# Performance work log

Measured on AMD Instinct MI355X. Metric: run time of the kernel, lower is better.

Reference implementation:

```python
import jax, jax.numpy as jnp
import numpy as np

KP_EXTENT = 0.05
N_Q = 40000   # query points
N_S = 40000   # support points
K = 32        # neighbors per query
P = 15        # kernel points
IN_DIM = 64
OUT_DIM = 128


def setup_inputs() -> dict:
    key = jax.random.key(0)
    k1, k2, k3, k4, k5, k6 = jax.random.split(key, 6)
    q_pts = jax.random.uniform(k1, (N_Q, 3), dtype=jnp.float32)
    s_pts = jax.random.uniform(k2, (N_S, 3), dtype=jnp.float32)
    # indices in [0, N_S]; value N_S hits the appended shadow row
    neighbor_idxs = jax.random.randint(k3, (N_Q, K), 0, N_S + 1)
    x = jax.random.normal(k4, (N_S, IN_DIM), dtype=jnp.float32)
    weights = jax.random.normal(k5, (P, IN_DIM, OUT_DIM), dtype=jnp.float32) * 0.05
    kernel_points = jax.random.normal(k6, (P, 3), dtype=jnp.float32) * 0.06
    return {"q_pts": q_pts, "s_pts": s_pts, "neighbor_idxs": neighbor_idxs,
            "x": x, "weights": weights, "kernel_points": kernel_points}


def reference(q_pts, s_pts, neighbor_idxs, x, weights, kernel_points):
    # Append shadow support point. NOTE: the original does
    # zeros_like(s_pts[:1,:] + 1e6) which is exactly zeros, so shadow = origin.
    s_pad = jnp.concatenate([s_pts, jnp.zeros_like(s_pts[:1, :])], axis=0)
    # Gather neighbor coordinates, center on queries: [N, K, 3]
    neighbors = s_pad[neighbor_idxs] - q_pts[:, None, :]
    # Distances to every kernel point: [N, K, P]
    diff = neighbors[:, :, None, :] - kernel_points[None, None, :, :]
    sq_distances = jnp.sum(diff * diff, axis=3)
    all_weights = jnp.clip(1.0 - jnp.sqrt(sq_distances) / KP_EXTENT, 0.0)
    all_weights = jnp.transpose(all_weights, (0, 2, 1))  # [N, P, K]
    # Gather neighbor features with zero shadow row: [N, K, D_in]
    feats = jnp.concatenate([x, jnp.zeros_like(x[:1, :])], axis=0)
    neighbors_x = feats[neighbor_idxs]
    # Kernel-point weighted aggregation: [N, P, D_in] -> [P, N, D_in]
    weighted_features = jnp.transpose(jnp.matmul(all_weights, neighbors_x), (1, 0, 2))
    # Per-kernel-point linear map: [P, N, D_out], then sum over kernel points
    kernel_outputs = jnp.matmul(weighted_features, weights)
    output_features = jnp.sum(kernel_outputs, axis=0)  # [N, D_out]
    # Normalize by count of "valid" neighbors (feature-sum > 0 heuristic)
    neighbor_features_sum = jnp.sum(neighbors_x, axis=-1)          # [N, K]
    neighbor_num = jnp.sum(neighbor_features_sum > 0.0, axis=-1)   # [N]
    neighbor_num = jnp.maximum(neighbor_num, 1).astype(output_features.dtype)
    return output_features / neighbor_num[:, None]
```

## Files before the change

### kernel.cpp

```cpp
#include <hip/hip_runtime.h>

#define N_Q     40000
#define N_S     40000
#define KK      32
#define PP      15
#define IN_DIM  64
#define OUT_DIM 128

__global__ __launch_bounds__(256) void rowsum_valid_kernel(
    const float* __restrict__ x, int* __restrict__ valid) {
  int t = blockIdx.x * 256 + threadIdx.x;
  int row = t >> 4;
  int sub = t & 15;
  if (row >= N_S) return;
  float4 v = reinterpret_cast<const float4*>(x + (size_t)row * IN_DIM)[sub];
  float s = (v.x + v.y) + (v.z + v.w);
  s += __shfl_xor(s, 1, 64);
  s += __shfl_xor(s, 2, 64);
  s += __shfl_xor(s, 4, 64);
  s += __shfl_xor(s, 8, 64);
  if (sub == 0) valid[row] = (s > 0.0f) ? 1 : 0;
}

__global__ __launch_bounds__(256) void kpconv_kernel(
    const float* __restrict__ q_pts, const float* __restrict__ s_pts,
    const int* __restrict__ nidx, const float* __restrict__ x,
    const float* __restrict__ weights, const float* __restrict__ kpts,
    const int* __restrict__ valid, float* __restrict__ out) {
  __shared__ float s_wf[4][PP * IN_DIM];
  __shared__ float s_nbr[4][KK * 3];
  __shared__ int   s_idx[4][KK];
  __shared__ int   s_pmask[4];
  __shared__ float s_kp[PP * 3];

  const int wave = threadIdx.x >> 6;
  const int lane = threadIdx.x & 63;
  const int n = blockIdx.x * 4 + wave;

  if (threadIdx.x < PP * 3) s_kp[threadIdx.x] = kpts[threadIdx.x];
  float* wf = s_wf[wave];
  for (int i = lane; i < PP * IN_DIM; i += 64) wf[i] = 0.0f;
  if (lane == 0) s_pmask[wave] = 0;

  const float qx = q_pts[n * 3 + 0];
  const float qy = q_pts[n * 3 + 1];
  const float qz = q_pts[n * 3 + 2];

  int cnt = 0;
  if (lane < KK) {
    int id = nidx[(size_t)n * KK + lane];
    s_idx[wave][lane] = id;
    float sx = 0.f, sy = 0.f, sz = 0.f;
    if (id < N_S) {
      sx = s_pts[id * 3 + 0];
      sy = s_pts[id * 3 + 1];
      sz = s_pts[id * 3 + 2];
      cnt = valid[id];
    }
    s_nbr[wave][lane * 3 + 0] = sx - qx;
    s_nbr[wave][lane * 3 + 1] = sy - qy;
    s_nbr[wave][lane * 3 + 2] = sz - qz;
  }
  unsigned long long bal = __ballot(cnt);
  int num = (int)__popcll(bal);
  if (num < 1) num = 1;
  const float fnum = (float)num;

  __syncthreads();

  for (int i = lane; i < PP * KK; i += 64) {
    const int p = i >> 5;
    const int k = i & 31;
    const float dx = s_nbr[wave][k * 3 + 0] - s_kp[p * 3 + 0];
    const float dy = s_nbr[wave][k * 3 + 1] - s_kp[p * 3 + 1];
    const float dz = s_nbr[wave][k * 3 + 2] - s_kp[p * 3 + 2];
    const float d2 = dx * dx + dy * dy + dz * dz;
    const float w = 1.0f - sqrtf(d2) * 20.0f;
    const int id = s_idx[wave][k];
    if (w > 0.0f && id < N_S) {
      atomicOr(&s_pmask[wave], 1 << p);
      const float4* f = reinterpret_cast<const float4*>(x + (size_t)id * IN_DIM);
      float* dst = wf + p * IN_DIM;
      #pragma unroll 4
      for (int d4 = 0; d4 < IN_DIM / 4; ++d4) {
        float4 v = f[d4];
        atomicAdd(&dst[d4 * 4 + 0], w * v.x);
        atomicAdd(&dst[d4 * 4 + 1], w * v.y);
        atomicAdd(&dst[d4 * 4 + 2], w * v.z);
        atomicAdd(&dst[d4 * 4 + 3], w * v.w);
      }
    }
  }
  __syncthreads();

  float acc0 = 0.f, acc1 = 0.f;
  int pmask = s_pmask[wave];
  const int o = lane * 2;
  while (pmask) {
    const int p = __ffs(pmask) - 1;
    pmask &= pmask - 1;
    const float* wp = weights + (size_t)p * IN_DIM * OUT_DIM + o;
    const float* wfp = wf + p * IN_DIM;
    #pragma unroll 8
    for (int d = 0; d < IN_DIM; ++d) {
      const float c = wfp[d];
      const float2 w2 = *reinterpret_cast<const float2*>(wp + (size_t)d * OUT_DIM);
      acc0 += c * w2.x;
      acc1 += c * w2.y;
    }
  }
  float2 res;
  res.x = acc0 / fnum;
  res.y = acc1 / fnum;
  *reinterpret_cast<float2*>(out + (size_t)n * OUT_DIM + o) = res;
}

extern "C" void kernel_launch(void* const* d_in, const int* in_sizes, int n_in,
                              void* d_out, int out_size, void* d_ws, size_t ws_size,
                              hipStream_t stream) {
  const float* q_pts   = (const float*)d_in[0];
  const float* s_pts   = (const float*)d_in[1];
  const int*   nidx    = (const int*)d_in[2];
  const float* x       = (const float*)d_in[3];
  const float* weights = (const float*)d_in[4];
  const float* kpts    = (const float*)d_in[5];
  float* out = (float*)d_out;
  int* valid = (int*)d_ws;

  rowsum_valid_kernel<<<(N_S * 16) / 256, 256, 0, stream>>>(x, valid);
  kpconv_kernel<<<N_Q / 4, 256, 0, stream>>>(q_pts, s_pts, nidx, x, weights,
                                             kpts, valid, out);
}
```

Measured before the change: 122.5 us.

## Parallelize over neighbor pairs and scatter sparse kernel-point contributions atomically

Each thread now handles one (query, neighbor) pair, testing the distance to every kernel point in registers. For each hit, the whole wave computes the neighbor's 64x128 projection via shuffles and atomically adds the scaled result into the zeroed output. This removes the per-query shared-memory zeroing, the barriers and the shared-memory atomics, relying on hits being sparse. It adds a memset and global float atomics, which change summation order, and work grows with hit density.

```diff
diff --git a/kernel.cpp b/kernel.cpp
--- a/kernel.cpp
+++ b/kernel.cpp
@@ -27,92 +27,67 @@
     const int* __restrict__ nidx, const float* __restrict__ x,
     const float* __restrict__ weights, const float* __restrict__ kpts,
     const int* __restrict__ valid, float* __restrict__ out) {
-  __shared__ float s_wf[4][PP * IN_DIM];
-  __shared__ float s_nbr[4][KK * 3];
-  __shared__ int   s_idx[4][KK];
-  __shared__ int   s_pmask[4];
-  __shared__ float s_kp[PP * 3];
+  const int tid  = blockIdx.x * 256 + threadIdx.x;
+  const int lane = threadIdx.x & 63;
+  const int n = tid >> 5;
+  const int k = tid & 31;
+  (void)k;
 
-  const int wave = threadIdx.x >> 6;
-  const int lane = threadIdx.x & 63;
-  const int n = blockIdx.x * 4 + wave;
+  const int id = nidx[tid];
 
-  if (threadIdx.x < PP * 3) s_kp[threadIdx.x] = kpts[threadIdx.x];
-  float* wf = s_wf[wave];
-  for (int i = lane; i < PP * IN_DIM; i += 64) wf[i] = 0.0f;
-  if (lane == 0) s_pmask[wave] = 0;
+  float ox = 0.f, oy = 0.f, oz = 0.f;
+  int v = 0;
+  if (id < N_S) {
+    ox = s_pts[id * 3 + 0];
+    oy = s_pts[id * 3 + 1];
+    oz = s_pts[id * 3 + 2];
+    v  = valid[id];
+  }
+  ox -= q_pts[n * 3 + 0];
+  oy -= q_pts[n * 3 + 1];
+  oz -= q_pts[n * 3 + 2];
 
-  const float qx = q_pts[n * 3 + 0];
-  const float qy = q_pts[n * 3 + 1];
-  const float qz = q_pts[n * 3 + 2];
+  unsigned long long bal = __ballot(v);
+  unsigned int half = (lane < 32) ? (unsigned int)bal
+                                  : (unsigned int)(bal >> 32);
+  int num = (int)__popc(half);
+  if (num < 1) num = 1;
+  const float invnum = 1.0f / (float)num;
 
-  int cnt = 0;
-  if (lane < KK) {
-    int id = nidx[(size_t)n * KK + lane];
-    s_idx[wave][lane] = id;
-    float sx = 0.f, sy = 0.f, sz = 0.f;
-    if (id < N_S) {
-      sx = s_pts[id * 3 + 0];
-      sy = s_pts[id * 3 + 1];
-      sz = s_pts[id * 3 + 2];
-      cnt = valid[id];
-    }
-    s_nbr[wave][lane * 3 + 0] = sx - qx;
-    s_nbr[wave][lane * 3 + 1] = sy - qy;
-    s_nbr[wave][lane * 3 + 2] = sz - qz;
-  }
-  unsigned long long bal = __ballot(cnt);
-  int num = (int)__popcll(bal);
-  if (num < 1) num = 1;
-  const float fnum = (float)num;
+  const bool real = (id < N_S);
 
-  __syncthreads();
+  for (int p = 0; p < PP; ++p) {
+    const float dx = ox - kpts[p * 3 + 0];
+    const float dy = oy - kpts[p * 3 + 1];
+    const float dz = oz - kpts[p * 3 + 2];
+    const float d2 = dx * dx + dy * dy + dz * dz;
+    const bool hit = real && (d2 < 0.0025f);
+    unsigned long long b2 = __ballot(hit);
+    if (b2 == 0ull) continue;
 
-  for (int i = lane; i < PP * KK; i += 64) {
-    const int p = i >> 5;
-    const int k = i & 31;
-    const float dx = s_nbr[wave][k * 3 + 0] - s_kp[p * 3 + 0];
-    const float dy = s_nbr[wave][k * 3 + 1] - s_kp[p * 3 + 1];
-    const float dz = s_nbr[wave][k * 3 + 2] - s_kp[p * 3 + 2];
-    const float d2 = dx * dx + dy * dy + dz * dz;
-    const float w = 1.0f - sqrtf(d2) * 20.0f;
-    const int id = s_idx[wave][k];
-    if (w > 0.0f && id < N_S) {
-      atomicOr(&s_pmask[wave], 1 << p);
-      const float4* f = reinterpret_cast<const float4*>(x + (size_t)id * IN_DIM);
-      float* dst = wf + p * IN_DIM;
-      #pragma unroll 4
-      for (int d4 = 0; d4 < IN_DIM / 4; ++d4) {
-        float4 v = f[d4];
-        atomicAdd(&dst[d4 * 4 + 0], w * v.x);
-        atomicAdd(&dst[d4 * 4 + 1], w * v.y);
-        atomicAdd(&dst[d4 * 4 + 2], w * v.z);
-        atomicAdd(&dst[d4 * 4 + 3], w * v.w);
+    const float wn = hit ? (1.0f - 20.0f * sqrtf(d2)) * invnum : 0.0f;
+
+    while (b2) {
+      const int j = __ffsll((unsigned long long)b2) - 1;
+      b2 &= b2 - 1;
+      const float wj  = __shfl(wn, j);
+      const int   idj = __shfl(id, j);
+      const int   nj  = __shfl(n,  j);
+
+      const float xv = x[(size_t)idj * IN_DIM + lane];
+      const float* wp = weights + (size_t)p * IN_DIM * OUT_DIM + 2 * lane;
+      float a0 = 0.f, a1 = 0.f;
+      #pragma unroll 16
+      for (int d = 0; d < IN_DIM; ++d) {
+        const float xd = __shfl(xv, d);
+        const float2 w2 = *reinterpret_cast<const float2*>(wp + (size_t)d * OUT_DIM);
+        a0 += xd * w2.x;
+        a1 += xd * w2.y;
       }
+      atomicAdd(&out[(size_t)nj * OUT_DIM + 2 * lane + 0], wj * a0);
+      atomicAdd(&out[(size_t)nj * OUT_DIM + 2 * lane + 1], wj * a1);
     }
   }
-  __syncthreads();
-
-  float acc0 = 0.f, acc1 = 0.f;
-  int pmask = s_pmask[wave];
-  const int o = lane * 2;
-  while (pmask) {
-    const int p = __ffs(pmask) - 1;
-    pmask &= pmask - 1;
-    const float* wp = weights + (size_t)p * IN_DIM * OUT_DIM + o;
-    const float* wfp = wf + p * IN_DIM;
-    #pragma unroll 8
-    for (int d = 0; d < IN_DIM; ++d) {
-      const float c = wfp[d];
-      const float2 w2 = *reinterpret_cast<const float2*>(wp + (size_t)d * OUT_DIM);
-      acc0 += c * w2.x;
-      acc1 += c * w2.y;
-    }
-  }
-  float2 res;
-  res.x = acc0 / fnum;
-  res.y = acc1 / fnum;
-  *reinterpret_cast<float2*>(out + (size_t)n * OUT_DIM + o) = res;
 }
 
 extern "C" void kernel_launch(void* const* d_in, const int* in_sizes, int n_in,
@@ -127,7 +102,8 @@
   float* out = (float*)d_out;
   int* valid = (int*)d_ws;
 
+  hipMemsetAsync(out, 0, (size_t)out_size * sizeof(float), stream);
   rowsum_valid_kernel<<<(N_S * 16) / 256, 256, 0, stream>>>(x, valid);
-  kpconv_kernel<<<N_Q / 4, 256, 0, stream>>>(q_pts, s_pts, nidx, x, weights,
-                                             kpts, valid, out);
+  kpconv_kernel<<<(N_Q * KK) / 256, 256, 0, stream>>>(
+      q_pts, s_pts, nidx, x, weights, kpts, valid, out);
 }
```

After: 120.4 us. Within noise of the previous version (-1.7%).
